# Performance work log

Measured on AMD Instinct MI355X. Metric: run time of the kernel, lower is better.

## Reference

```python
import jax, jax.numpy as jnp
import numpy as np

ALPHA = 0.65  # self.alpha
B, L = 4096, 4096


def setup_inputs() -> dict:
    key = jax.random.key(0)
    k1, k2 = jax.random.split(key)
    output = jax.random.normal(k1, (B, L, 2), dtype=jnp.float32)
    labels = jax.random.randint(k2, (B, L), 0, 2, dtype=jnp.int32)
    return {"output": output, "labels": labels}


def reference(output, labels):
    # output: [B, L, 2] (channel 0 = truncate, channel 1 = continue); labels: [B, L] in {0,1}
    Bn, Ln, _ = output.shape
    # --- slice_index, vectorized over the batch ---
    temp = jnp.argmax(output, axis=-1)                    # [B, L] in {0,1}
    all_ones = jnp.all(temp == 1, axis=1)                 # [B]
    # index of the last 0 in temp[i]: L-1 - (first-min index of the flipped row)
    k = jnp.argmin(temp[:, ::-1], axis=1)                 # [B]
    cut = jnp.where(all_ones, Ln, Ln - 1 - k)             # [B]; mask[i, cut:] = 0
    mask = (jnp.arange(Ln)[None, :] < cut[:, None]).astype(output.dtype)  # [B, L]
    # --- reward tensor r (metric='nci'): r[...,0] = 0 always, r[...,1] depends on label ---
    j = jnp.arange(Ln, dtype=output.dtype)
    pos_reward = -3.6 / jnp.log2(j + 2.0)                 # [L]
    r1 = jnp.where(labels == 1, pos_reward[None, :], ALPHA * 0.1)  # [B, L]
    # sum(output * mask * r) / B; only channel 1 contributes since r[...,0] == 0
    loss = jnp.sum(output[..., 1] * mask * r1) / Bn
    return loss
```

## Files before the change

kernel.cpp:

```cpp
#include <hip/hip_runtime.h>


#define LROW 4096
#define BROW 4096
#define BDIM 256
#define PAIRS_PER_THREAD (LROW / (2 * BDIM))

__global__ __launch_bounds__(BDIM) void bicut_loss_kernel(
    const float* __restrict__ out,
    const int* __restrict__ labels,
    float* __restrict__ loss) {
    const int row = blockIdx.x;
    const int tid = threadIdx.x;
    const float4* rowp4 = reinterpret_cast<const float4*>(out + (size_t)row * LROW * 2);
    const int2* labp2 = reinterpret_cast<const int2*>(labels + (size_t)row * LROW);

    float val0[PAIRS_PER_THREAD];
    float val1[PAIRS_PER_THREAD];
    int zmax = -1;
#pragma unroll
    for (int it = 0; it < PAIRS_PER_THREAD; ++it) {
        const int p = it * BDIM + tid;
        const float4 o = rowp4[p];
        const int2 lab = labp2[p];
        const int j0 = 2 * p;
        const int j1 = 2 * p + 1;
        const float pr0 = -3.6f / __log2f((float)j0 + 2.0f);
        const float pr1 = -3.6f / __log2f((float)j1 + 2.0f);
        val0[it] = o.y * ((lab.x == 1) ? pr0 : 0.065f);
        val1[it] = o.w * ((lab.y == 1) ? pr1 : 0.065f);
        if (!(o.y > o.x)) zmax = j0;
        if (!(o.w > o.z)) zmax = j1;
    }

    __shared__ int smax[BDIM / 64];
    __shared__ float ssum[BDIM / 64];
    const int wid = tid >> 6;
    const int lane = tid & 63;
#pragma unroll
    for (int off = 32; off > 0; off >>= 1)
        zmax = max(zmax, __shfl_down(zmax, off));
    if (lane == 0) smax[wid] = zmax;
    __syncthreads();
    const int m01 = max(smax[0], smax[1]);
    const int m23 = max(smax[2], smax[3]);
    const int mall = max(m01, m23);
    const int cut = (mall < 0) ? LROW : mall;

    float s = 0.0f;
#pragma unroll
    for (int it = 0; it < PAIRS_PER_THREAD; ++it) {
        const int p = it * BDIM + tid;
        const int j0 = 2 * p;
        const int j1 = 2 * p + 1;
        if (j0 < cut) s += val0[it];
        if (j1 < cut) s += val1[it];
    }
#pragma unroll
    for (int off = 32; off > 0; off >>= 1)
        s += __shfl_down(s, off);
    if (lane == 0) ssum[wid] = s;
    __syncthreads();
    if (tid == 0) {
        const float bs = (ssum[0] + ssum[1] + ssum[2] + ssum[3]) * (1.0f / (float)BROW);
        atomicAdd(loss, bs);
    }
}

extern "C" void kernel_launch(void* const* d_in, const int* in_sizes, int n_in,
                              void* d_out, int out_size, void* d_ws, size_t ws_size,
                              hipStream_t stream) {
    const float* out = (const float*)d_in[0];
    const int* labels = (const int*)d_in[1];
    float* loss = (float*)d_out;

    hipMemsetAsync(loss, 0, sizeof(float), stream);
    bicut_loss_kernel<<<BROW, BDIM, 0, stream>>>(out, labels, loss);
}
```

Baseline: 234.3 us.

## Replace atomic accumulation with per-row partials and a final reduction kernel

Each row block now writes its partial sum to workspace, and a second single-block kernel reduces those partials, replacing the memset and the global atomicAdd. The block size doubles to 512 threads, and all row loads are issued up front before compute so more memory traffic is in flight. The division is replaced with a hardware reciprocal. The cost is an extra kernel launch, and the reciprocal may differ slightly in precision.

```diff
diff --git a/kernel.cpp b/kernel.cpp
--- a/kernel.cpp
+++ b/kernel.cpp
@@ -3,68 +3,92 @@
 
 #define LROW 4096
 #define BROW 4096
-#define BDIM 256
-#define PAIRS_PER_THREAD (LROW / (2 * BDIM))
+#define BDIM 512
+#define NPAIRS (LROW / 2)
+#define K_ITERS (NPAIRS / BDIM)
 
-__global__ __launch_bounds__(BDIM) void bicut_loss_kernel(
+__global__ __launch_bounds__(BDIM) void bicut_partial_kernel(
     const float* __restrict__ out,
     const int* __restrict__ labels,
-    float* __restrict__ loss) {
+    float* __restrict__ partial) {
     const int row = blockIdx.x;
     const int tid = threadIdx.x;
     const float4* rowp4 = reinterpret_cast<const float4*>(out + (size_t)row * LROW * 2);
     const int2* labp2 = reinterpret_cast<const int2*>(labels + (size_t)row * LROW);
 
-    float val0[PAIRS_PER_THREAD];
-    float val1[PAIRS_PER_THREAD];
+    float4 o[K_ITERS];
+    int2 lb[K_ITERS];
+#pragma unroll
+    for (int k = 0; k < K_ITERS; ++k) {
+        const int p = k * BDIM + tid;
+        o[k] = rowp4[p];
+        lb[k] = labp2[p];
+    }
+
+    float v0[K_ITERS], v1[K_ITERS];
     int zmax = -1;
 #pragma unroll
-    for (int it = 0; it < PAIRS_PER_THREAD; ++it) {
-        const int p = it * BDIM + tid;
-        const float4 o = rowp4[p];
-        const int2 lab = labp2[p];
-        const int j0 = 2 * p;
-        const int j1 = 2 * p + 1;
-        const float pr0 = -3.6f / __log2f((float)j0 + 2.0f);
-        const float pr1 = -3.6f / __log2f((float)j1 + 2.0f);
-        val0[it] = o.y * ((lab.x == 1) ? pr0 : 0.065f);
-        val1[it] = o.w * ((lab.y == 1) ? pr1 : 0.065f);
-        if (!(o.y > o.x)) zmax = j0;
-        if (!(o.w > o.z)) zmax = j1;
+    for (int k = 0; k < K_ITERS; ++k) {
+        const int p = k * BDIM + tid;
+        const int j0 = 2 * p, j1 = j0 + 1;
+        const float pr0 = -3.6f * __builtin_amdgcn_rcpf(__log2f((float)j0 + 2.0f));
+        const float pr1 = -3.6f * __builtin_amdgcn_rcpf(__log2f((float)j1 + 2.0f));
+        v0[k] = o[k].y * ((lb[k].x == 1) ? pr0 : 0.065f);
+        v1[k] = o[k].w * ((lb[k].y == 1) ? pr1 : 0.065f);
+        if (!(o[k].y > o[k].x)) zmax = j0;
+        if (!(o[k].w > o[k].z)) zmax = j1;
     }
 
     __shared__ int smax[BDIM / 64];
     __shared__ float ssum[BDIM / 64];
-    const int wid = tid >> 6;
-    const int lane = tid & 63;
+    const int wid = tid >> 6, lane = tid & 63;
 #pragma unroll
-    for (int off = 32; off > 0; off >>= 1)
-        zmax = max(zmax, __shfl_down(zmax, off));
+    for (int off = 32; off; off >>= 1) zmax = max(zmax, __shfl_down(zmax, off));
     if (lane == 0) smax[wid] = zmax;
     __syncthreads();
-    const int m01 = max(smax[0], smax[1]);
-    const int m23 = max(smax[2], smax[3]);
-    const int mall = max(m01, m23);
+    int mall = smax[0];
+#pragma unroll
+    for (int w = 1; w < BDIM / 64; ++w) mall = max(mall, smax[w]);
     const int cut = (mall < 0) ? LROW : mall;
 
     float s = 0.0f;
 #pragma unroll
-    for (int it = 0; it < PAIRS_PER_THREAD; ++it) {
-        const int p = it * BDIM + tid;
-        const int j0 = 2 * p;
-        const int j1 = 2 * p + 1;
-        if (j0 < cut) s += val0[it];
-        if (j1 < cut) s += val1[it];
+    for (int k = 0; k < K_ITERS; ++k) {
+        const int p = k * BDIM + tid;
+        const int j0 = 2 * p, j1 = j0 + 1;
+        if (j0 < cut) s += v0[k];
+        if (j1 < cut) s += v1[k];
     }
 #pragma unroll
-    for (int off = 32; off > 0; off >>= 1)
-        s += __shfl_down(s, off);
+    for (int off = 32; off; off >>= 1) s += __shfl_down(s, off);
     if (lane == 0) ssum[wid] = s;
     __syncthreads();
     if (tid == 0) {
-        const float bs = (ssum[0] + ssum[1] + ssum[2] + ssum[3]) * (1.0f / (float)BROW);
-        atomicAdd(loss, bs);
+        float bs = 0.0f;
+#pragma unroll
+        for (int w = 0; w < BDIM / 64; ++w) bs += ssum[w];
+        partial[row] = bs;
     }
+}
+
+__global__ __launch_bounds__(256) void bicut_final_kernel(
+    const float* __restrict__ partial,
+    float* __restrict__ loss) {
+    const int tid = threadIdx.x;
+    const float4* p4 = reinterpret_cast<const float4*>(partial);
+    float s = 0.0f;
+#pragma unroll
+    for (int k = 0; k < BROW / 4 / 256; ++k) {
+        const float4 v = p4[k * 256 + tid];
+        s += v.x + v.y + v.z + v.w;
+    }
+    __shared__ float ss[4];
+    const int wid = tid >> 6, lane = tid & 63;
+#pragma unroll
+    for (int off = 32; off; off >>= 1) s += __shfl_down(s, off);
+    if (lane == 0) ss[wid] = s;
+    __syncthreads();
+    if (tid == 0) loss[0] = (ss[0] + ss[1] + ss[2] + ss[3]) * (1.0f / (float)BROW);
 }
 
 extern "C" void kernel_launch(void* const* d_in, const int* in_sizes, int n_in,
@@ -73,7 +97,8 @@
     const float* out = (const float*)d_in[0];
     const int* labels = (const int*)d_in[1];
     float* loss = (float*)d_out;
+    float* partial = (float*)d_ws;
 
-    hipMemsetAsync(loss, 0, sizeof(float), stream);
-    bicut_loss_kernel<<<BROW, BDIM, 0, stream>>>(out, labels, loss);
+    bicut_partial_kernel<<<BROW, BDIM, 0, stream>>>(out, labels, partial);
+    bicut_final_kernel<<<1, 256, 0, stream>>>(partial, loss);
 }
```

Result: no change. 230.3 us (-1.7%).
